# Kernel optimization log

Hardware: AMD Instinct MI355X
Metric: run time of the kernel (lower is better)

## Reference

```python
import jax, jax.numpy as jnp
import numpy as np

H = 128
B = 512
T = 1024
FUT = 64


def setup_inputs() -> dict:
    key = jax.random.key(0)
    ks = jax.random.split(key, 11)
    k = 1.0 / np.sqrt(H)  # torch LSTMCell/Linear init range
    u = lambda kk, shape: jax.random.uniform(kk, shape, jnp.float32, -k, k)
    return {
        "x": jax.random.normal(ks[0], (B, T), jnp.float32),
        "W_ih1": u(ks[1], (4 * H, 1)),
        "b_ih1": u(ks[2], (4 * H,)),
        "W_hh1": u(ks[3], (4 * H, H)),
        "b_hh1": u(ks[4], (4 * H,)),
        "W_ih2": u(ks[5], (4 * H, H)),
        "b_ih2": u(ks[6], (4 * H,)),
        "W_hh2": u(ks[7], (4 * H, H)),
        "b_hh2": u(ks[8], (4 * H,)),
        "W_out": u(ks[9], (1, H)),
        "b_out": u(ks[10], (1,)),
        "future": FUT,
    }


def _cell(x_t, h, c, W_ih, b_ih, W_hh, b_hh):
    # torch.nn.LSTMCell: gates ordered i, f, g, o
    g = x_t @ W_ih.T + h @ W_hh.T + (b_ih + b_hh)
    i, f, gg, o = jnp.split(g, 4, axis=-1)
    c_new = jax.nn.sigmoid(f) * c + jax.nn.sigmoid(i) * jnp.tanh(gg)
    h_new = jax.nn.sigmoid(o) * jnp.tanh(c_new)
    return h_new, c_new


def reference(x, W_ih1, b_ih1, W_hh1, b_hh1, W_ih2, b_ih2, W_hh2, b_hh2, W_out, b_out, future):
    Bn = x.shape[0]
    Hn = W_hh1.shape[1]
    z = jnp.zeros((Bn, Hn), x.dtype)

    def enc_step(carry, x_t):
        h1, c1, h2, c2 = carry
        h1, c1 = _cell(x_t, h1, c1, W_ih1, b_ih1, W_hh1, b_hh1)
        h2, c2 = _cell(h1, h2, c2, W_ih2, b_ih2, W_hh2, b_hh2)
        return (h1, c1, h2, c2), None

    xs = x.T[:, :, None]  # [T, B, 1]
    (h1, c1, h2, c2), _ = jax.lax.scan(enc_step, (z, z, z, z), xs)
    out0 = h2 @ W_out.T + b_out  # [B, 1]

    def fut_step(carry, _):
        h1, c1, h2, c2, out = carry
        h1, c1 = _cell(out, h1, c1, W_ih1, b_ih1, W_hh1, b_hh1)
        h2, c2 = _cell(h1, h2, c2, W_ih2, b_ih2, W_hh2, b_hh2)
        out = h2 @ W_out.T + b_out
        return (h1, c1, h2, c2, out), out

    _, fouts = jax.lax.scan(fut_step, (h1, c1, h2, c2, out0), None, length=future - 1)
    # torch cats [B,1] tensors on dim=1 -> [B, future]
    return jnp.concatenate([out0, fouts[:, :, 0].T], axis=1)
```

## Files before the change

kernel.cpp:

```cpp
#include <hip/hip_runtime.h>

#define HH 128
#define TT 1024
#define NFUT 64
#define MB 2
#define NBLK 256

typedef _Float16 half8 __attribute__((ext_vector_type(8)));
typedef float floatx4 __attribute__((ext_vector_type(4)));

#define MFMA16(a, b, c) __builtin_amdgcn_mfma_f32_16x16x32_f16((a), (b), (c), 0, 0, 0)

__device__ __forceinline__ float sigm(float v) {
  return __builtin_amdgcn_rcpf(1.0f + __builtin_amdgcn_exp2f(v * -1.442695040888963f));
}
__device__ __forceinline__ float tanh_f(float v) {
  float a = __builtin_fabsf(v);
  float e = __builtin_amdgcn_exp2f(a * -2.885390081777927f);
  float r = (1.0f - e) * __builtin_amdgcn_rcpf(1.0f + e);
  return __builtin_copysignf(r, v);
}

__device__ __forceinline__ half8 ldw8(const float* __restrict__ p) {
  half8 r;
#pragma unroll
  for (int i = 0; i < 8; ++i) r[i] = (_Float16)p[i];
  return r;
}

__global__ __launch_bounds__(512, 2) void lstm_kernel(
    const float* __restrict__ x,
    const float* __restrict__ W_ih1, const float* __restrict__ b_ih1,
    const float* __restrict__ W_hh1, const float* __restrict__ b_hh1,
    const float* __restrict__ W_ih2, const float* __restrict__ b_ih2,
    const float* __restrict__ W_hh2, const float* __restrict__ b_hh2,
    const float* __restrict__ W_out, const float* __restrict__ b_out,
    float* __restrict__ out)
{
  __shared__ __align__(16) _Float16 xs[TT * 16];
  __shared__ __align__(16) _Float16 h1b[2 * 2048];
  __shared__ __align__(16) _Float16 h2b[2 * 2048];
  __shared__ float oscr[8 * 16];
  __shared__ float xfut[16];

  const int tid = (int)threadIdx.x;
  const int lane = tid & 63;
  const int w = tid >> 6;
  const int jl = lane & 15;
  const int rg = lane >> 4;
  const int j = (w << 4) + jl;
  const int b0g = (int)blockIdx.x * MB;

  for (int idx = tid; idx < TT * 16; idx += 512) {
    int b = idx >> 10;
    int t = idx & (TT - 1);
    float v = (b < MB) ? x[(b0g + b) * TT + t] : 0.0f;
    xs[t * 16 + b] = (_Float16)v;
  }
  for (int i = tid; i < 2 * 2048; i += 512) {
    h1b[i] = (_Float16)0.0f;
    h2b[i] = (_Float16)0.0f;
  }

  half8 fr1[4][4], f2i[4][4], f2h[4][4];
#pragma unroll
  for (int q = 0; q < 4; ++q) {
#pragma unroll
    for (int kf = 0; kf < 4; ++kf) {
      int row = q * HH + j;
      int kb = kf * 32 + rg * 8;
      fr1[q][kf] = ldw8(W_hh1 + row * HH + kb);
      f2i[q][kf] = ldw8(W_ih2 + row * HH + kb);
      f2h[q][kf] = ldw8(W_hh2 + row * HH + kb);
    }
  }
  float bias1[4], bias2[4], wi1[4];
#pragma unroll
  for (int q = 0; q < 4; ++q) {
    bias1[q] = b_ih1[q * HH + j] + b_hh1[q * HH + j];
    bias2[q] = b_ih2[q * HH + j] + b_hh2[q * HH + j];
    wi1[q] = W_ih1[q * HH + j];
  }
  const float wo = W_out[j];
  const float bo = b_out[0];

  floatx4 c1 = {0.0f, 0.0f, 0.0f, 0.0f};
  floatx4 c2 = {0.0f, 0.0f, 0.0f, 0.0f};

  __syncthreads();

  const int aoff = lane * 8;
  const int wconst = ((j >> 5) << 9) + (((j >> 3) & 3) << 7) + (j & 7);

  for (int t = 0; t < TT + NFUT - 1; ++t) {
    const int cur = (t & 1);
    const _Float16* h1c = h1b + cur * 2048;
    _Float16* h1n = h1b + (cur ^ 1) * 2048;
    const _Float16* h2c = h2b + cur * 2048;
    _Float16* h2n = h2b + (cur ^ 1) * 2048;

    floatx4 a0 = {0,0,0,0}, a1 = {0,0,0,0}, a2 = {0,0,0,0}, a3 = {0,0,0,0};
#pragma unroll
    for (int kf = 0; kf < 4; ++kf) {
      half8 av = *(const half8*)(h1c + (kf << 9) + aoff);
      a0 = MFMA16(av, fr1[0][kf], a0);
      a1 = MFMA16(av, fr1[1][kf], a1);
      a2 = MFMA16(av, fr1[2][kf], a2);
      a3 = MFMA16(av, fr1[3][kf], a3);
    }

    float xv[4];
    if (t < TT) {
#pragma unroll
      for (int r = 0; r < 4; ++r) xv[r] = (float)xs[t * 16 + rg * 4 + r];
    } else {
#pragma unroll
      for (int r = 0; r < 4; ++r) xv[r] = xfut[rg * 4 + r];
    }
#pragma unroll
    for (int r = 0; r < 4; ++r) {
      if (rg * 4 + r < MB) {
        float gi = a0[r] + xv[r] * wi1[0] + bias1[0];
        float gf = a1[r] + xv[r] * wi1[1] + bias1[1];
        float gg = a2[r] + xv[r] * wi1[2] + bias1[2];
        float go = a3[r] + xv[r] * wi1[3] + bias1[3];
        float cc = sigm(gf) * c1[r] + sigm(gi) * tanh_f(gg);
        c1[r] = cc;
        float hh = sigm(go) * tanh_f(cc);
        h1n[wconst + ((rg * 4 + r) << 3)] = (_Float16)hh;
      }
    }
    __syncthreads();

    floatx4 g0 = {0,0,0,0}, g1 = {0,0,0,0}, g2 = {0,0,0,0}, g3 = {0,0,0,0};
#pragma unroll
    for (int kf = 0; kf < 4; ++kf) {
      half8 av = *(const half8*)(h2c + (kf << 9) + aoff);
      g0 = MFMA16(av, f2h[0][kf], g0);
      g1 = MFMA16(av, f2h[1][kf], g1);
      g2 = MFMA16(av, f2h[2][kf], g2);
      g3 = MFMA16(av, f2h[3][kf], g3);
    }
#pragma unroll
    for (int kf = 0; kf < 4; ++kf) {
      half8 av = *(const half8*)(h1n + (kf << 9) + aoff);
      g0 = MFMA16(av, f2i[0][kf], g0);
      g1 = MFMA16(av, f2i[1][kf], g1);
      g2 = MFMA16(av, f2i[2][kf], g2);
      g3 = MFMA16(av, f2i[3][kf], g3);
    }

    float hvr[4] = {0.0f, 0.0f, 0.0f, 0.0f};
#pragma unroll
    for (int r = 0; r < 4; ++r) {
      if (rg * 4 + r < MB) {
        float gi = g0[r] + bias2[0];
        float gf = g1[r] + bias2[1];
        float gg = g2[r] + bias2[2];
        float go = g3[r] + bias2[3];
        float cc = sigm(gf) * c2[r] + sigm(gi) * tanh_f(gg);
        c2[r] = cc;
        float hh = sigm(go) * tanh_f(cc);
        h2n[wconst + ((rg * 4 + r) << 3)] = (_Float16)hh;
        hvr[r] = hh;
      }
    }

    if (t >= TT - 1) {
      if (rg == 0) {
#pragma unroll
        for (int r = 0; r < MB; ++r) {
          float p = hvr[r] * wo;
          p += __shfl_xor(p, 1);
          p += __shfl_xor(p, 2);
          p += __shfl_xor(p, 4);
          p += __shfl_xor(p, 8);
          if (jl == 0) oscr[w * 16 + r] = p;
        }
      }
      __syncthreads();
      if (tid < MB) {
        float s = bo;
#pragma unroll
        for (int ww = 0; ww < 8; ++ww) s += oscr[ww * 16 + tid];
        out[(b0g + tid) * NFUT + (t - (TT - 1))] = s;
        xfut[tid] = s;
      }
    }
    __syncthreads();
  }
}

extern "C" void kernel_launch(void* const* d_in, const int* in_sizes, int n_in,
                              void* d_out, int out_size, void* d_ws, size_t ws_size,
                              hipStream_t stream) {
  const float* x     = (const float*)d_in[0];
  const float* W_ih1 = (const float*)d_in[1];
  const float* b_ih1 = (const float*)d_in[2];
  const float* W_hh1 = (const float*)d_in[3];
  const float* b_hh1 = (const float*)d_in[4];
  const float* W_ih2 = (const float*)d_in[5];
  const float* b_ih2 = (const float*)d_in[6];
  const float* W_hh2 = (const float*)d_in[7];
  const float* b_hh2 = (const float*)d_in[8];
  const float* W_out = (const float*)d_in[9];
  const float* b_out = (const float*)d_in[10];
  (void)in_sizes; (void)n_in; (void)out_size; (void)d_ws; (void)ws_size;

  lstm_kernel<<<dim3(NBLK), dim3(512), 0, stream>>>(
      x, W_ih1, b_ih1, W_hh1, b_hh1, W_ih2, b_ih2, W_hh2, b_hh2, W_out, b_out,
      (float*)d_out);
}
```

Baseline: 1.809 ms.

## Split LSTM layers across wavefront groups and pipeline them with one barrier per step

Each block now runs 1024 threads. Waves 0-7 compute layer 1 and waves 8-15 compute layer 2 for the previous timestep, so the two layers run concurrently as a skewed pipeline. During the encoder phase this leaves one barrier per step instead of two. Gate values are redistributed with lane shuffles so only 32 lanes do the activation math, and the x staging buffer shrinks to two batch rows. The cost is one resident block per CU, half of the waves idle in the serial chain at each step, and an extra barrier during the future-prediction phase.

```diff
diff --git a/kernel.cpp b/kernel.cpp
--- a/kernel.cpp
+++ b/kernel.cpp
@@ -5,6 +5,7 @@
 #define NFUT 64
 #define MB 2
 #define NBLK 256
+#define NITER (TT + NFUT)
 
 typedef _Float16 half8 __attribute__((ext_vector_type(8)));
 typedef float floatx4 __attribute__((ext_vector_type(4)));
@@ -20,7 +21,6 @@
   float r = (1.0f - e) * __builtin_amdgcn_rcpf(1.0f + e);
   return __builtin_copysignf(r, v);
 }
-
 __device__ __forceinline__ half8 ldw8(const float* __restrict__ p) {
   half8 r;
 #pragma unroll
@@ -28,7 +28,7 @@
   return r;
 }
 
-__global__ __launch_bounds__(512, 2) void lstm_kernel(
+__global__ __launch_bounds__(1024, 1) void lstm_kernel(
     const float* __restrict__ x,
     const float* __restrict__ W_ih1, const float* __restrict__ b_ih1,
     const float* __restrict__ W_hh1, const float* __restrict__ b_hh1,
@@ -37,154 +37,153 @@
     const float* __restrict__ W_out, const float* __restrict__ b_out,
     float* __restrict__ out)
 {
-  __shared__ __align__(16) _Float16 xs[TT * 16];
-  __shared__ __align__(16) _Float16 h1b[2 * 2048];
-  __shared__ __align__(16) _Float16 h2b[2 * 2048];
-  __shared__ float oscr[8 * 16];
-  __shared__ float xfut[16];
+  __shared__ __align__(16) _Float16 h1b[2][2048];
+  __shared__ __align__(16) _Float16 h2b[2][2048];
+  __shared__ __align__(16) _Float16 xs[TT * MB];
+  __shared__ float opart[8 * 4];
 
   const int tid = (int)threadIdx.x;
   const int lane = tid & 63;
   const int w = tid >> 6;
+  const bool isC1 = (w < 8);
+  const int nw = w & 7;
   const int jl = lane & 15;
   const int rg = lane >> 4;
-  const int j = (w << 4) + jl;
-  const int b0g = (int)blockIdx.x * MB;
-
-  for (int idx = tid; idx < TT * 16; idx += 512) {
-    int b = idx >> 10;
+  const int j = nw * 16 + jl;
+  const int b0 = (int)blockIdx.x * MB;
+
+  for (int idx = tid; idx < TT * MB; idx += 1024) {
     int t = idx & (TT - 1);
-    float v = (b < MB) ? x[(b0g + b) * TT + t] : 0.0f;
-    xs[t * 16 + b] = (_Float16)v;
-  }
-  for (int i = tid; i < 2 * 2048; i += 512) {
-    h1b[i] = (_Float16)0.0f;
-    h2b[i] = (_Float16)0.0f;
-  }
-
-  half8 fr1[4][4], f2i[4][4], f2h[4][4];
-#pragma unroll
-  for (int q = 0; q < 4; ++q) {
-#pragma unroll
-    for (int kf = 0; kf < 4; ++kf) {
-      int row = q * HH + j;
-      int kb = kf * 32 + rg * 8;
-      fr1[q][kf] = ldw8(W_hh1 + row * HH + kb);
-      f2i[q][kf] = ldw8(W_ih2 + row * HH + kb);
-      f2h[q][kf] = ldw8(W_hh2 + row * HH + kb);
-    }
-  }
-  float bias1[4], bias2[4], wi1[4];
-#pragma unroll
-  for (int q = 0; q < 4; ++q) {
-    bias1[q] = b_ih1[q * HH + j] + b_hh1[q * HH + j];
-    bias2[q] = b_ih2[q * HH + j] + b_hh2[q * HH + j];
-    wi1[q] = W_ih1[q * HH + j];
-  }
-  const float wo = W_out[j];
+    int bb = idx >> 10;
+    xs[t * MB + bb] = (_Float16)x[(b0 + bb) * TT + t];
+  }
+  for (int idx = tid; idx < 2 * 2048; idx += 1024) {
+    h1b[idx >> 11][idx & 2047] = (_Float16)0.0f;
+    h2b[idx >> 11][idx & 2047] = (_Float16)0.0f;
+  }
+
+  half8 wf[8][4];
+  float bias[4], wi1[4] = {0.f, 0.f, 0.f, 0.f};
+  float wo = 0.f;
+  if (isC1) {
+#pragma unroll
+    for (int q = 0; q < 4; ++q) {
+#pragma unroll
+      for (int kf = 0; kf < 4; ++kf)
+        wf[q][kf] = ldw8(W_hh1 + (q * HH + j) * HH + kf * 32 + rg * 8);
+      bias[q] = b_ih1[q * HH + j] + b_hh1[q * HH + j];
+      wi1[q] = W_ih1[q * HH + j];
+    }
+  } else {
+#pragma unroll
+    for (int q = 0; q < 4; ++q) {
+#pragma unroll
+      for (int kf = 0; kf < 4; ++kf) {
+        wf[q][kf]     = ldw8(W_hh2 + (q * HH + j) * HH + kf * 32 + rg * 8);
+        wf[4 + q][kf] = ldw8(W_ih2 + (q * HH + j) * HH + kf * 32 + rg * 8);
+      }
+      bias[q] = b_ih2[q * HH + j] + b_hh2[q * HH + j];
+    }
+    wo = W_out[j];
+  }
   const float bo = b_out[0];
-
-  floatx4 c1 = {0.0f, 0.0f, 0.0f, 0.0f};
-  floatx4 c2 = {0.0f, 0.0f, 0.0f, 0.0f};
+  float c = 0.f;
 
   __syncthreads();
 
   const int aoff = lane * 8;
-  const int wconst = ((j >> 5) << 9) + (((j >> 3) & 3) << 7) + (j & 7);
-
-  for (int t = 0; t < TT + NFUT - 1; ++t) {
-    const int cur = (t & 1);
-    const _Float16* h1c = h1b + cur * 2048;
-    _Float16* h1n = h1b + (cur ^ 1) * 2048;
-    const _Float16* h2c = h2b + cur * 2048;
-    _Float16* h2n = h2b + (cur ^ 1) * 2048;
-
-    floatx4 a0 = {0,0,0,0}, a1 = {0,0,0,0}, a2 = {0,0,0,0}, a3 = {0,0,0,0};
-#pragma unroll
-    for (int kf = 0; kf < 4; ++kf) {
-      half8 av = *(const half8*)(h1c + (kf << 9) + aoff);
-      a0 = MFMA16(av, fr1[0][kf], a0);
-      a1 = MFMA16(av, fr1[1][kf], a1);
-      a2 = MFMA16(av, fr1[2][kf], a2);
-      a3 = MFMA16(av, fr1[3][kf], a3);
-    }
-
-    float xv[4];
-    if (t < TT) {
-#pragma unroll
-      for (int r = 0; r < 4; ++r) xv[r] = (float)xs[t * 16 + rg * 4 + r];
-    } else {
-#pragma unroll
-      for (int r = 0; r < 4; ++r) xv[r] = xfut[rg * 4 + r];
-    }
-#pragma unroll
-    for (int r = 0; r < 4; ++r) {
-      if (rg * 4 + r < MB) {
-        float gi = a0[r] + xv[r] * wi1[0] + bias1[0];
-        float gf = a1[r] + xv[r] * wi1[1] + bias1[1];
-        float gg = a2[r] + xv[r] * wi1[2] + bias1[2];
-        float go = a3[r] + xv[r] * wi1[3] + bias1[3];
-        float cc = sigm(gf) * c1[r] + sigm(gi) * tanh_f(gg);
-        c1[r] = cc;
-        float hh = sigm(go) * tanh_f(cc);
-        h1n[wconst + ((rg * 4 + r) << 3)] = (_Float16)hh;
-      }
-    }
-    __syncthreads();
-
-    floatx4 g0 = {0,0,0,0}, g1 = {0,0,0,0}, g2 = {0,0,0,0}, g3 = {0,0,0,0};
-#pragma unroll
-    for (int kf = 0; kf < 4; ++kf) {
-      half8 av = *(const half8*)(h2c + (kf << 9) + aoff);
-      g0 = MFMA16(av, f2h[0][kf], g0);
-      g1 = MFMA16(av, f2h[1][kf], g1);
-      g2 = MFMA16(av, f2h[2][kf], g2);
-      g3 = MFMA16(av, f2h[3][kf], g3);
-    }
-#pragma unroll
-    for (int kf = 0; kf < 4; ++kf) {
-      half8 av = *(const half8*)(h1n + (kf << 9) + aoff);
-      g0 = MFMA16(av, f2i[0][kf], g0);
-      g1 = MFMA16(av, f2i[1][kf], g1);
-      g2 = MFMA16(av, f2i[2][kf], g2);
-      g3 = MFMA16(av, f2i[3][kf], g3);
-    }
-
-    float hvr[4] = {0.0f, 0.0f, 0.0f, 0.0f};
-#pragma unroll
-    for (int r = 0; r < 4; ++r) {
-      if (rg * 4 + r < MB) {
-        float gi = g0[r] + bias2[0];
-        float gf = g1[r] + bias2[1];
-        float gg = g2[r] + bias2[2];
-        float go = g3[r] + bias2[3];
-        float cc = sigm(gf) * c2[r] + sigm(gi) * tanh_f(gg);
-        c2[r] = cc;
-        float hh = sigm(go) * tanh_f(cc);
-        h2n[wconst + ((rg * 4 + r) << 3)] = (_Float16)hh;
-        hvr[r] = hh;
-      }
-    }
-
-    if (t >= TT - 1) {
-      if (rg == 0) {
-#pragma unroll
-        for (int r = 0; r < MB; ++r) {
-          float p = hvr[r] * wo;
+  const int wbase = ((j >> 5) << 9) + (((j >> 3) & 3) << 7) + (j & 7) + ((lane >> 4) << 3);
+
+  for (int i = 0; i < NITER; ++i) {
+    const int cur = i & 1;
+    floatx4 acc[4] = {{0.f,0.f,0.f,0.f},{0.f,0.f,0.f,0.f},{0.f,0.f,0.f,0.f},{0.f,0.f,0.f,0.f}};
+
+    if (isC1) {
+      if (i < NITER - 1) {
+#pragma unroll
+        for (int kf = 0; kf < 4; ++kf) {
+          half8 av = *(const half8*)(&h1b[cur][kf * 512 + aoff]);
+          acc[0] = MFMA16(av, wf[0][kf], acc[0]);
+          acc[1] = MFMA16(av, wf[1][kf], acc[1]);
+          acc[2] = MFMA16(av, wf[2][kf], acc[2]);
+          acc[3] = MFMA16(av, wf[3][kf], acc[3]);
+        }
+      }
+    } else if (i >= 1) {
+#pragma unroll
+      for (int kf = 0; kf < 4; ++kf) {
+        half8 av = *(const half8*)(&h2b[cur][kf * 512 + aoff]);
+        acc[0] = MFMA16(av, wf[0][kf], acc[0]);
+        acc[1] = MFMA16(av, wf[1][kf], acc[1]);
+        acc[2] = MFMA16(av, wf[2][kf], acc[2]);
+        acc[3] = MFMA16(av, wf[3][kf], acc[3]);
+      }
+#pragma unroll
+      for (int kf = 0; kf < 4; ++kf) {
+        half8 av = *(const half8*)(&h1b[cur][kf * 512 + aoff]);
+        acc[0] = MFMA16(av, wf[4][kf], acc[0]);
+        acc[1] = MFMA16(av, wf[5][kf], acc[1]);
+        acc[2] = MFMA16(av, wf[6][kf], acc[2]);
+        acc[3] = MFMA16(av, wf[7][kf], acc[3]);
+      }
+      float g[4];
+#pragma unroll
+      for (int q = 0; q < 4; ++q) {
+        float t0 = __shfl(acc[q][0], jl);
+        float t1 = __shfl(acc[q][1], jl);
+        g[q] = (lane & 16) ? t1 : t0;
+      }
+      if (lane < 32) {
+        float gi = g[0] + bias[0];
+        float gf = g[1] + bias[1];
+        float gg = g[2] + bias[2];
+        float go = g[3] + bias[3];
+        c = sigm(gf) * c + sigm(gi) * tanh_f(gg);
+        float h = sigm(go) * tanh_f(c);
+        h2b[cur ^ 1][wbase] = (_Float16)h;
+        if (i >= TT) {
+          float p = h * wo;
           p += __shfl_xor(p, 1);
           p += __shfl_xor(p, 2);
           p += __shfl_xor(p, 4);
           p += __shfl_xor(p, 8);
-          if (jl == 0) oscr[w * 16 + r] = p;
-        }
-      }
-      __syncthreads();
-      if (tid < MB) {
-        float s = bo;
-#pragma unroll
-        for (int ww = 0; ww < 8; ++ww) s += oscr[ww * 16 + tid];
-        out[(b0g + tid) * NFUT + (t - (TT - 1))] = s;
-        xfut[tid] = s;
+          if (jl == 0) opart[nw * MB + (lane >> 4)] = p;
+        }
+      }
+    }
+
+    if (i >= TT) __syncthreads();
+
+    if (isC1) {
+      float xv = 0.f;
+      if (lane < 32) {
+        if (i < TT) {
+          xv = (float)xs[i * MB + (lane >> 4)];
+        } else {
+          float s = bo;
+#pragma unroll
+          for (int p8 = 0; p8 < 8; ++p8) s += opart[p8 * MB + (lane >> 4)];
+          xv = s;
+          if (w == 0 && jl == 0) out[(b0 + (lane >> 4)) * NFUT + (i - TT)] = s;
+        }
+      }
+      if (i < NITER - 1) {
+        float g[4];
+#pragma unroll
+        for (int q = 0; q < 4; ++q) {
+          float t0 = __shfl(acc[q][0], jl);
+          float t1 = __shfl(acc[q][1], jl);
+          g[q] = (lane & 16) ? t1 : t0;
+        }
+        if (lane < 32) {
+          float gi = g[0] + xv * wi1[0] + bias[0];
+          float gf = g[1] + xv * wi1[1] + bias[1];
+          float gg = g[2] + xv * wi1[2] + bias[2];
+          float go = g[3] + xv * wi1[3] + bias[3];
+          c = sigm(gf) * c + sigm(gi) * tanh_f(gg);
+          float h = sigm(go) * tanh_f(c);
+          h1b[cur ^ 1][wbase] = (_Float16)h;
+        }
       }
     }
     __syncthreads();
@@ -207,7 +206,7 @@
   const float* b_out = (const float*)d_in[10];
   (void)in_sizes; (void)n_in; (void)out_size; (void)d_ws; (void)ws_size;
 
-  lstm_kernel<<<dim3(NBLK), dim3(512), 0, stream>>>(
+  lstm_kernel<<<dim3(NBLK), dim3(1024), 0, stream>>>(
       x, W_ih1, b_ih1, W_hh1, b_hh1, W_ih2, b_ih2, W_hh2, b_hh2, W_out, b_out,
       (float*)d_out);
 }
```

Result: slower. 3.355 ms (+85.5%).
